# Optimization experiments

Hardware: AMD Instinct MI355X
Metric: run time of the kernel (lower is better)

## Reference

```python
import jax, jax.numpy as jnp
import numpy as np

N = 6            # fixed by nn.Linear(6, h2) after the transpose/squeeze
NEG_SLOPE = 0.01 # F.leaky_relu default


def setup_inputs() -> dict:
    key = jax.random.key(0)
    ks = jax.random.split(key, 12)
    B, H1, H2, H3 = 131072, 64, 512, 256
    in_feat = jax.random.normal(ks[0], (N, B, 1), dtype=jnp.float32)
    # deterministic bidirectional ring: every node has in/out degree 2 (norm='both' safe)
    ar = jnp.arange(N, dtype=jnp.int32)
    src = jnp.concatenate([ar, ar])
    dst = jnp.concatenate([(ar + 1) % N, (ar - 1) % N]).astype(jnp.int32)
    s = 0.2
    W0  = jax.random.normal(ks[1], (1, H1), jnp.float32) * s
    b0  = jax.random.normal(ks[2], (H1,), jnp.float32) * s
    W1  = jax.random.normal(ks[3], (H1, 1), jnp.float32) * s
    b1  = jax.random.normal(ks[4], (1,), jnp.float32) * s
    Wl0 = jax.random.normal(ks[5], (N, H2), jnp.float32) * s
    bl0 = jax.random.normal(ks[6], (H2,), jnp.float32) * s
    Wl2 = jax.random.normal(ks[7], (H2, H3), jnp.float32) * s
    bl2 = jax.random.normal(ks[8], (H3,), jnp.float32) * s
    Wl3 = jax.random.normal(ks[9], (H3, 1), jnp.float32) * s
    bl3 = jax.random.normal(ks[10], (1,), jnp.float32) * s
    return {"in_feat": in_feat, "src": src, "dst": dst,
            "W0": W0, "b0": b0, "W1": W1, "b1": b1,
            "Wl0": Wl0, "bl0": bl0, "Wl2": Wl2, "bl2": bl2,
            "Wl3": Wl3, "bl3": bl3}


def _lrelu(x):
    return jnp.where(x >= 0, x, NEG_SLOPE * x)


def _degree_norms(src, dst):
    ones = jnp.ones(src.shape[0], dtype=jnp.float32)
    deg_out = jax.ops.segment_sum(ones, src, num_segments=N)
    deg_in = jax.ops.segment_sum(ones, dst, num_segments=N)
    return deg_out ** -0.5, deg_in ** -0.5  # DGL GraphConv norm='both'


def _graph_conv(feat, W, b, src, dst, inv_out, inv_in):
    # D_out^{-1/2} A^T D_in^{-1/2} feat  then linear (order is math-equivalent)
    h = feat * inv_out[:, None, None]           # [N,B,F]
    agg = jax.ops.segment_sum(h[src], dst, num_segments=N)  # gather+scatter over edges
    agg = agg * inv_in[:, None, None]
    return agg @ W + b


def reference(in_feat, src, dst, W0, b0, W1, b1, Wl0, bl0, Wl2, bl2, Wl3, bl3):
    inv_out, inv_in = _degree_norms(src, dst)
    h = _lrelu(_graph_conv(in_feat, W0, b0, src, dst, inv_out, inv_in))  # [N,B,h1]
    h = _lrelu(_graph_conv(h, W1, b1, src, dst, inv_out, inv_in))        # [N,B,1]
    x = jnp.transpose(h, (2, 1, 0))[0]   # transpose(0,2).squeeze(0) -> [B,N]
    x = _lrelu(x @ Wl0 + bl0)
    x = _lrelu(x @ Wl2 + bl2)
    x = _lrelu(x @ Wl3 + bl3)            # [B,1]; squeeze(0) is a no-op for B>1
    return x
```

## Files before the change

### kernel.cpp

```cpp
#include <hip/hip_runtime.h>

#define NN   6
#define H1   64
#define H2   512
#define H3   256
#define TM   256
#define KC   32
#define NCH  (H2 / KC)
#define CHUNK_BYTES 32768

typedef short s16x8 __attribute__((ext_vector_type(8)));
typedef float f32x16 __attribute__((ext_vector_type(16)));

__device__ __forceinline__ unsigned short f2bf(float x) {
    unsigned int u = __float_as_uint(x);
    u += 0x7FFFu + ((u >> 16) & 1u);
    return (unsigned short)(u >> 16);
}
__device__ __forceinline__ float bf2f(unsigned short b) {
    return __uint_as_float(((unsigned int)b) << 16);
}
__device__ __forceinline__ void g2lds16(const void* g, void* l) {
    __builtin_amdgcn_global_load_lds(
        (const __attribute__((address_space(1))) unsigned int*)g,
        (__attribute__((address_space(3))) unsigned int*)l, 16, 0, 0);
}

__global__ void split_w(const float* __restrict__ Wl2,
                        unsigned short* __restrict__ Whl) {
    const int tid = blockIdx.x * 256 + threadIdx.x;
    const int c0 = tid >> 13, q = tid & 8191;
    const int j = q & 7, col = (q >> 3) & 255, th = q >> 11;
    const int k = (c0 << 5) + (th << 3) + j;
    const float w = Wl2[k * H3 + col];
    const unsigned short hi = f2bf(w);
    const unsigned short lo = f2bf(w - bf2f(hi));
    Whl[(c0 << 14) + q] = hi;
    Whl[(c0 << 14) + 8192 + q] = lo;
}

__global__ __launch_bounds__(512, 2)
void gcn_mfma(const float* __restrict__ f,
              const float* __restrict__ W0,
              const float* __restrict__ b0,
              const float* __restrict__ W1,
              const float* __restrict__ b1_,
              const float* __restrict__ Wl0,
              const float* __restrict__ bl0,
              const float* __restrict__ bl2,
              const float* __restrict__ Wl3,
              const float* __restrict__ bl3_,
              const unsigned short* __restrict__ Whl,
              float* __restrict__ out,
              int B)
{
    __shared__ float sW0[H1], sB0[H1], sW1[H1];
    __shared__ float sWl0[NN][H2];
    __shared__ float sBl0[H2];
    __shared__ float sBl2[H3];
    __shared__ float sWl3[H3];
    __shared__ float sF[NN][TM];
    __shared__ float sS[NN][TM];
    __shared__ float sX[NN][TM];
    __shared__ __align__(16) unsigned short sB[2][16384];

    const int t    = threadIdx.x;
    const int lane = t & 63;
    const int w    = t >> 6;
    const int cl   = lane & 31;
    const int h    = lane >> 5;
    const int m0   = blockIdx.x * TM;

    for (int i = t; i < H1; i += 512) { sW0[i] = W0[i]; sB0[i] = b0[i]; sW1[i] = W1[i]; }
    for (int i = t; i < NN * H2; i += 512) sWl0[i >> 9][i & (H2 - 1)] = Wl0[i];
    for (int i = t; i < H2; i += 512) sBl0[i] = bl0[i];
    for (int i = t; i < H3; i += 512) { sBl2[i] = bl2[i]; sWl3[i] = Wl3[i]; }
    for (int i = t; i < NN * TM; i += 512) sF[i >> 8][i & 255] = f[(i >> 8) * B + m0 + (i & 255)];

    {
        const char* src = (const char*)Whl + (w << 12) + (lane << 4);
        char*       dst = (char*)&sB[0][0] + (w << 12);
        #pragma unroll
        for (int q = 0; q < 4; ++q) g2lds16(src + (q << 10), dst + (q << 10));
    }
    __syncthreads();

    const float b1v = b1_[0];

    for (int v = t; v < NN * TM; v += 512) {
        const int i = v >> 8, r = v & 255;
        const int im = (i + NN - 1) % NN, ip = (i + 1) % NN;
        const float g = 0.5f * (sF[im][r] + sF[ip][r]);
        float s = 0.f;
        #pragma unroll
        for (int c = 0; c < H1; ++c) {
            float hx = g * sW0[c] + sB0[c];
            hx = fmaxf(hx, 0.01f * hx);
            s += hx * sW1[c];
        }
        sS[i][r] = s;
    }
    __syncthreads();
    for (int v = t; v < NN * TM; v += 512) {
        const int i = v >> 8, r = v & 255;
        const int im = (i + NN - 1) % NN, ip = (i + 1) % NN;
        const float xv = 0.5f * (sS[im][r] + sS[ip][r]) + b1v;
        sX[i][r] = fmaxf(xv, 0.01f * xv);
    }
    __syncthreads();

    const int myrow = (w << 5) + cl;
    const float x0 = sX[0][myrow], x1 = sX[1][myrow], x2 = sX[2][myrow],
                x3 = sX[3][myrow], x4 = sX[4][myrow], x5 = sX[5][myrow];

    f32x16 acc[8];
    #pragma unroll
    for (int c = 0; c < 8; ++c)
        #pragma unroll
        for (int rg = 0; rg < 16; ++rg) acc[c][rg] = 0.f;

    for (int ch = 0; ch < NCH; ++ch) {
        const int cur = ch & 1;
        if (ch + 1 < NCH) {
            const char* src = (const char*)Whl + (ch + 1) * CHUNK_BYTES + (w << 12) + (lane << 4);
            char*       dst = (char*)&sB[cur ^ 1][0] + (w << 12);
            #pragma unroll
            for (int q = 0; q < 4; ++q) g2lds16(src + (q << 10), dst + (q << 10));
        }
        #pragma unroll
        for (int tt = 0; tt < 2; ++tt) {
            const int k0 = (ch << 5) + (tt << 4) + (h << 3);
            float4 va = *(const float4*)&sBl0[k0];
            float4 vb = *(const float4*)&sBl0[k0 + 4];
            #pragma unroll
            for (int i = 0; i < 6; ++i) {
                const float xi = (i == 0) ? x0 : (i == 1) ? x1 : (i == 2) ? x2
                               : (i == 3) ? x3 : (i == 4) ? x4 : x5;
                const float4 wa = *(const float4*)&sWl0[i][k0];
                const float4 wb = *(const float4*)&sWl0[i][k0 + 4];
                va.x += xi * wa.x; va.y += xi * wa.y; va.z += xi * wa.z; va.w += xi * wa.w;
                vb.x += xi * wb.x; vb.y += xi * wb.y; vb.z += xi * wb.z; vb.w += xi * wb.w;
            }
            float vv[8] = {va.x, va.y, va.z, va.w, vb.x, vb.y, vb.z, vb.w};
            s16x8 ah, al;
            #pragma unroll
            for (int j = 0; j < 8; ++j) {
                float v = vv[j];
                v = fmaxf(v, 0.01f * v);
                const unsigned short hb = f2bf(v);
                const unsigned short lb = f2bf(v - bf2f(hb));
                ah[j] = (short)hb;
                al[j] = (short)lb;
            }
            const int thh = (tt << 1) + h;
            s16x8 bh[8];
            #pragma unroll
            for (int c = 0; c < 8; ++c)
                bh[c] = *(const s16x8*)&sB[cur][(((0 + thh) * 256) + (c << 5) + cl) << 3];
            #pragma unroll
            for (int c = 0; c < 8; ++c)
                acc[c] = __builtin_amdgcn_mfma_f32_32x32x16_bf16(ah, bh[c], acc[c], 0, 0, 0);
            #pragma unroll
            for (int c = 0; c < 8; ++c)
                acc[c] = __builtin_amdgcn_mfma_f32_32x32x16_bf16(al, bh[c], acc[c], 0, 0, 0);
            #pragma unroll
            for (int c = 0; c < 8; ++c) {
                const s16x8 bl = *(const s16x8*)&sB[cur][(((4 + thh) * 256) + (c << 5) + cl) << 3];
                acc[c] = __builtin_amdgcn_mfma_f32_32x32x16_bf16(ah, bl, acc[c], 0, 0, 0);
            }
        }
        __syncthreads();
    }

    float ps[16];
    #pragma unroll
    for (int rg = 0; rg < 16; ++rg) ps[rg] = 0.f;
    #pragma unroll
    for (int c = 0; c < 8; ++c) {
        const int col = (c << 5) + cl;
        const float b2 = sBl2[col], w3 = sWl3[col];
        #pragma unroll
        for (int rg = 0; rg < 16; ++rg) {
            float v = acc[c][rg] + b2;
            v = fmaxf(v, 0.01f * v);
            ps[rg] += v * w3;
        }
    }
    #pragma unroll
    for (int m = 1; m < 32; m <<= 1)
        #pragma unroll
        for (int rg = 0; rg < 16; ++rg) ps[rg] += __shfl_xor(ps[rg], m);
    if (cl == 0) {
        const float bl3v = bl3_[0];
        #pragma unroll
        for (int rg = 0; rg < 16; ++rg) {
            const int row = (rg & 3) + ((rg >> 2) << 3) + (h << 2);
            const float v = ps[rg] + bl3v;
            out[m0 + (w << 5) + row] = fmaxf(v, 0.01f * v);
        }
    }
}

extern "C" void kernel_launch(void* const* d_in, const int* in_sizes, int n_in,
                              void* d_out, int out_size, void* d_ws, size_t ws_size,
                              hipStream_t stream) {
    const float* f   = (const float*)d_in[0];
    const float* W0  = (const float*)d_in[3];
    const float* b0  = (const float*)d_in[4];
    const float* W1  = (const float*)d_in[5];
    const float* b1  = (const float*)d_in[6];
    const float* Wl0 = (const float*)d_in[7];
    const float* bl0 = (const float*)d_in[8];
    const float* Wl2 = (const float*)d_in[9];
    const float* bl2 = (const float*)d_in[10];
    const float* Wl3 = (const float*)d_in[11];
    const float* bl3 = (const float*)d_in[12];
    float* out = (float*)d_out;
    unsigned short* Whl = (unsigned short*)d_ws;
    const int B = in_sizes[0] / NN;

    split_w<<<dim3(H2 * H3 / 256), 256, 0, stream>>>(Wl2, Whl);
    gcn_mfma<<<dim3(B / TM), 512, 0, stream>>>(f, W0, b0, W1, b1, Wl0, bl0,
                                               bl2, Wl3, bl3, Whl, out, B);
}
```

Before: 195.0 us.

## Software-pipeline A-fragment generation ahead of MFMAs with packed bf16 conversion

Unrolls the chunk loop by two with fixed double-buffer indices and computes the next chunk's A-operand (first-layer linear, leaky ReLU, hi/lo bf16 split) before issuing the MFMAs for the current chunk. This lets VALU work overlap matrix-core work. It also swaps the scalar bf16 rounding for the packed v_cvt_pk_bf16_f32 instruction and uses 2-wide float vector math. B-fragment loads are split into groups of four to reduce live registers, but the extra prefetched A fragments raise register pressure, which risks occupancy at 2 blocks of 512 threads.

```diff
diff --git a/kernel.cpp b/kernel.cpp
--- a/kernel.cpp
+++ b/kernel.cpp
@@ -11,6 +11,8 @@
 
 typedef short s16x8 __attribute__((ext_vector_type(8)));
 typedef float f32x16 __attribute__((ext_vector_type(16)));
+typedef float f32x2 __attribute__((ext_vector_type(2)));
+typedef unsigned int u32x4 __attribute__((ext_vector_type(4)));
 
 __device__ __forceinline__ unsigned short f2bf(float x) {
     unsigned int u = __float_as_uint(x);
@@ -19,6 +21,11 @@
 }
 __device__ __forceinline__ float bf2f(unsigned short b) {
     return __uint_as_float(((unsigned int)b) << 16);
+}
+__device__ __forceinline__ unsigned int cvt_pk_bf16(float a, float b) {
+    unsigned int r;
+    asm("v_cvt_pk_bf16_f32 %0, %1, %2" : "=v"(r) : "v"(a), "v"(b));
+    return r;
 }
 __device__ __forceinline__ void g2lds16(const void* g, void* l) {
     __builtin_amdgcn_global_load_lds(
@@ -77,12 +84,14 @@
     for (int i = t; i < H3; i += 512) { sBl2[i] = bl2[i]; sWl3[i] = Wl3[i]; }
     for (int i = t; i < NN * TM; i += 512) sF[i >> 8][i & 255] = f[(i >> 8) * B + m0 + (i & 255)];
 
-    {
-        const char* src = (const char*)Whl + (w << 12) + (lane << 4);
-        char*       dst = (char*)&sB[0][0] + (w << 12);
-        #pragma unroll
-        for (int q = 0; q < 4; ++q) g2lds16(src + (q << 10), dst + (q << 10));
-    }
+#define STAGE(CH, BUF) do {                                                        \
+        const char* _src = (const char*)Whl + (CH) * CHUNK_BYTES + (w << 12) + (lane << 4); \
+        char*       _dst = (char*)&sB[BUF][0] + (w << 12);                         \
+        _Pragma("unroll")                                                          \
+        for (int _q = 0; _q < 4; ++_q) g2lds16(_src + (_q << 10), _dst + (_q << 10)); \
+    } while (0)
+
+    STAGE(0, 0);
     __syncthreads();
 
     const float b1v = b1_[0];
@@ -110,8 +119,9 @@
     __syncthreads();
 
     const int myrow = (w << 5) + cl;
-    const float x0 = sX[0][myrow], x1 = sX[1][myrow], x2 = sX[2][myrow],
-                x3 = sX[3][myrow], x4 = sX[4][myrow], x5 = sX[5][myrow];
+    float xr[NN];
+    #pragma unroll
+    for (int i = 0; i < NN; ++i) xr[i] = sX[i][myrow];
 
     f32x16 acc[8];
     #pragma unroll
@@ -119,56 +129,78 @@
         #pragma unroll
         for (int rg = 0; rg < 16; ++rg) acc[c][rg] = 0.f;
 
-    for (int ch = 0; ch < NCH; ++ch) {
-        const int cur = ch & 1;
-        if (ch + 1 < NCH) {
-            const char* src = (const char*)Whl + (ch + 1) * CHUNK_BYTES + (w << 12) + (lane << 4);
-            char*       dst = (char*)&sB[cur ^ 1][0] + (w << 12);
-            #pragma unroll
-            for (int q = 0; q < 4; ++q) g2lds16(src + (q << 10), dst + (q << 10));
-        }
-        #pragma unroll
-        for (int tt = 0; tt < 2; ++tt) {
-            const int k0 = (ch << 5) + (tt << 4) + (h << 3);
-            float4 va = *(const float4*)&sBl0[k0];
-            float4 vb = *(const float4*)&sBl0[k0 + 4];
-            #pragma unroll
-            for (int i = 0; i < 6; ++i) {
-                const float xi = (i == 0) ? x0 : (i == 1) ? x1 : (i == 2) ? x2
-                               : (i == 3) ? x3 : (i == 4) ? x4 : x5;
-                const float4 wa = *(const float4*)&sWl0[i][k0];
-                const float4 wb = *(const float4*)&sWl0[i][k0 + 4];
-                va.x += xi * wa.x; va.y += xi * wa.y; va.z += xi * wa.z; va.w += xi * wa.w;
-                vb.x += xi * wb.x; vb.y += xi * wb.y; vb.z += xi * wb.z; vb.w += xi * wb.w;
-            }
-            float vv[8] = {va.x, va.y, va.z, va.w, vb.x, vb.y, vb.z, vb.w};
-            s16x8 ah, al;
-            #pragma unroll
-            for (int j = 0; j < 8; ++j) {
-                float v = vv[j];
-                v = fmaxf(v, 0.01f * v);
-                const unsigned short hb = f2bf(v);
-                const unsigned short lb = f2bf(v - bf2f(hb));
-                ah[j] = (short)hb;
-                al[j] = (short)lb;
-            }
-            const int thh = (tt << 1) + h;
-            s16x8 bh[8];
-            #pragma unroll
-            for (int c = 0; c < 8; ++c)
-                bh[c] = *(const s16x8*)&sB[cur][(((0 + thh) * 256) + (c << 5) + cl) << 3];
-            #pragma unroll
-            for (int c = 0; c < 8; ++c)
-                acc[c] = __builtin_amdgcn_mfma_f32_32x32x16_bf16(ah, bh[c], acc[c], 0, 0, 0);
-            #pragma unroll
-            for (int c = 0; c < 8; ++c)
-                acc[c] = __builtin_amdgcn_mfma_f32_32x32x16_bf16(al, bh[c], acc[c], 0, 0, 0);
-            #pragma unroll
-            for (int c = 0; c < 8; ++c) {
-                const s16x8 bl = *(const s16x8*)&sB[cur][(((4 + thh) * 256) + (c << 5) + cl) << 3];
-                acc[c] = __builtin_amdgcn_mfma_f32_32x32x16_bf16(ah, bl, acc[c], 0, 0, 0);
-            }
-        }
+#define K0(CH, TT) (((CH) << 5) + ((TT) << 4) + (h << 3))
+#define GEN_TT(K0V, AH, AL) do {                                                   \
+        const int _k0 = (K0V);                                                     \
+        f32x2 _ac[4];                                                              \
+        _Pragma("unroll")                                                          \
+        for (int _j = 0; _j < 4; ++_j) _ac[_j] = *(const f32x2*)&sBl0[_k0 + 2*_j]; \
+        _Pragma("unroll")                                                          \
+        for (int _i = 0; _i < 6; ++_i) {                                           \
+            const float _xi = xr[_i];                                              \
+            _Pragma("unroll")                                                      \
+            for (int _j = 0; _j < 4; ++_j)                                         \
+                _ac[_j] += _xi * (*(const f32x2*)&sWl0[_i][_k0 + 2*_j]);           \
+        }                                                                          \
+        unsigned int _hw[4], _lw[4];                                               \
+        _Pragma("unroll")                                                          \
+        for (int _j = 0; _j < 4; ++_j) {                                           \
+            f32x2 _v = _ac[_j];                                                    \
+            _v = __builtin_elementwise_max(_v, 0.01f * _v);                        \
+            const unsigned int _uh = cvt_pk_bf16(_v[0], _v[1]);                    \
+            f32x2 _hf = { __uint_as_float(_uh << 16),                              \
+                          __uint_as_float(_uh & 0xFFFF0000u) };                    \
+            const f32x2 _r = _v - _hf;                                             \
+            _hw[_j] = _uh; _lw[_j] = cvt_pk_bf16(_r[0], _r[1]);                    \
+        }                                                                          \
+        const u32x4 _u4 = {_hw[0], _hw[1], _hw[2], _hw[3]};                        \
+        const u32x4 _l4 = {_lw[0], _lw[1], _lw[2], _lw[3]};                        \
+        AH = __builtin_bit_cast(s16x8, _u4);                                       \
+        AL = __builtin_bit_cast(s16x8, _l4);                                       \
+    } while (0)
+
+#define MFMA_TT(SBC, TT, AH, AL) do {                                              \
+        const int _thh = ((TT) << 1) + h;                                          \
+        const unsigned short* _bb = &(SBC)[((_thh << 8) + cl) << 3];               \
+        _Pragma("unroll")                                                          \
+        for (int _g = 0; _g < 2; ++_g) {                                           \
+            s16x8 _bh[4];                                                          \
+            _Pragma("unroll")                                                      \
+            for (int _i = 0; _i < 4; ++_i)                                         \
+                _bh[_i] = *(const s16x8*)&_bb[(_g * 4 + _i) << 8];                 \
+            _Pragma("unroll")                                                      \
+            for (int _i = 0; _i < 4; ++_i)                                         \
+                acc[_g*4+_i] = __builtin_amdgcn_mfma_f32_32x32x16_bf16(AH, _bh[_i], acc[_g*4+_i], 0, 0, 0); \
+            _Pragma("unroll")                                                      \
+            for (int _i = 0; _i < 4; ++_i)                                         \
+                acc[_g*4+_i] = __builtin_amdgcn_mfma_f32_32x32x16_bf16(AL, _bh[_i], acc[_g*4+_i], 0, 0, 0); \
+            _Pragma("unroll")                                                      \
+            for (int _i = 0; _i < 4; ++_i) {                                       \
+                const s16x8 _bl = *(const s16x8*)&_bb[8192 + ((_g * 4 + _i) << 8)];\
+                acc[_g*4+_i] = __builtin_amdgcn_mfma_f32_32x32x16_bf16(AH, _bl, acc[_g*4+_i], 0, 0, 0); \
+            }                                                                      \
+        }                                                                          \
+    } while (0)
+
+    s16x8 ahA0, alA0, ahA1, alA1;
+    s16x8 ahB0, alB0, ahB1, alB1;
+    GEN_TT(K0(0, 0), ahA0, alA0);
+    GEN_TT(K0(0, 1), ahA1, alA1);
+
+    for (int ch = 0; ch < NCH; ch += 2) {
+        STAGE(ch + 1, 1);
+        GEN_TT(K0(ch + 1, 0), ahB0, alB0);
+        GEN_TT(K0(ch + 1, 1), ahB1, alB1);
+        MFMA_TT((&sB[0][0]), 0, ahA0, alA0);
+        MFMA_TT((&sB[0][0]), 1, ahA1, alA1);
+        __syncthreads();
+        if (ch + 2 < NCH) {
+            STAGE(ch + 2, 0);
+            GEN_TT(K0(ch + 2, 0), ahA0, alA0);
+            GEN_TT(K0(ch + 2, 1), ahA1, alA1);
+        }
+        MFMA_TT((&sB[1][0]), 0, ahB0, alB0);
+        MFMA_TT((&sB[1][0]), 1, ahB1, alB1);
         __syncthreads();
     }
 
```

Measured after the change: 182.9 us. -6.2%, faster.

## Retile MFMA warps as 2x2 row/col blocks and software-pipeline A-fragment generation

Applied to the files above, without the earlier changes.

Each warp now computes 64 rows by 128 columns instead of 32 rows by 256 columns. This halves the number of A-fragments generated per warp relative to its output work and lets each B-fragment load from LDS feed two MFMAs. The chunk loop is unrolled by two with explicit double buffers, so the layer-1 activations for the next chunk are computed while the current chunk's MFMAs run. The bf16 hi/lo split now uses packed v_cvt_pk_bf16_f32, and split_w reads the weights with float4 loads. The final reduction goes through shared memory across the two column-warps, and the extra live fragments add register pressure.

```diff
diff --git a/kernel.cpp b/kernel.cpp
--- a/kernel.cpp
+++ b/kernel.cpp
@@ -11,6 +11,8 @@
 
 typedef short s16x8 __attribute__((ext_vector_type(8)));
 typedef float f32x16 __attribute__((ext_vector_type(16)));
+typedef float f32x2 __attribute__((ext_vector_type(2)));
+typedef unsigned int u32x4 __attribute__((ext_vector_type(4)));
 
 __device__ __forceinline__ unsigned short f2bf(float x) {
     unsigned int u = __float_as_uint(x);
@@ -20,6 +22,11 @@
 __device__ __forceinline__ float bf2f(unsigned short b) {
     return __uint_as_float(((unsigned int)b) << 16);
 }
+__device__ __forceinline__ unsigned int cvt_pk_bf16(float a, float b) {
+    unsigned int r;
+    asm("v_cvt_pk_bf16_f32 %0, %1, %2" : "=v"(r) : "v"(a), "v"(b));
+    return r;
+}
 __device__ __forceinline__ void g2lds16(const void* g, void* l) {
     __builtin_amdgcn_global_load_lds(
         (const __attribute__((address_space(1))) unsigned int*)g,
@@ -28,15 +35,59 @@
 
 __global__ void split_w(const float* __restrict__ Wl2,
                         unsigned short* __restrict__ Whl) {
-    const int tid = blockIdx.x * 256 + threadIdx.x;
-    const int c0 = tid >> 13, q = tid & 8191;
-    const int j = q & 7, col = (q >> 3) & 255, th = q >> 11;
-    const int k = (c0 << 5) + (th << 3) + j;
-    const float w = Wl2[k * H3 + col];
-    const unsigned short hi = f2bf(w);
-    const unsigned short lo = f2bf(w - bf2f(hi));
-    Whl[(c0 << 14) + q] = hi;
-    Whl[(c0 << 14) + 8192 + q] = lo;
+    const int gid = blockIdx.x * 256 + threadIdx.x;
+    const int k = gid >> 6, c4 = (gid & 63) << 2;
+    const float4 v = *(const float4*)&Wl2[k * H3 + c4];
+    const int c0 = k >> 5, th = (k >> 3) & 3, j = k & 7;
+    const unsigned base = (c0 << 14) + (th << 11) + j;
+    const float vv[4] = {v.x, v.y, v.z, v.w};
+    #pragma unroll
+    for (int c = 0; c < 4; ++c) {
+        const unsigned short hi = f2bf(vv[c]);
+        const unsigned short lo = f2bf(vv[c] - bf2f(hi));
+        Whl[base + ((c4 + c) << 3)] = hi;
+        Whl[base + 8192 + ((c4 + c) << 3)] = lo;
+    }
+}
+
+__device__ __forceinline__ void gen2(const float* sBl0s, const float (*sWl0s)[H2],
+                                     int k0, const float* xr0, const float* xr1,
+                                     s16x8& ah0, s16x8& al0, s16x8& ah1, s16x8& al1)
+{
+    f32x2 a0[4], a1[4];
+    #pragma unroll
+    for (int j = 0; j < 4; ++j) {
+        const f32x2 b = *(const f32x2*)&sBl0s[k0 + 2 * j];
+        f32x2 c0 = b, c1 = b;
+        #pragma unroll
+        for (int i = 0; i < 6; ++i) {
+            const f32x2 wv = *(const f32x2*)&sWl0s[i][k0 + 2 * j];
+            c0 += xr0[i] * wv;
+            c1 += xr1[i] * wv;
+        }
+        a0[j] = c0; a1[j] = c1;
+    }
+    unsigned int h0[4], l0[4], h1[4], l1[4];
+    #pragma unroll
+    for (int j = 0; j < 4; ++j) {
+        f32x2 v = a0[j];
+        v = __builtin_elementwise_max(v, 0.01f * v);
+        unsigned int u = cvt_pk_bf16(v[0], v[1]);
+        f32x2 hf = { __uint_as_float(u << 16), __uint_as_float(u & 0xFFFF0000u) };
+        f32x2 r = v - hf;
+        h0[j] = u; l0[j] = cvt_pk_bf16(r[0], r[1]);
+        v = a1[j];
+        v = __builtin_elementwise_max(v, 0.01f * v);
+        u = cvt_pk_bf16(v[0], v[1]);
+        hf = (f32x2){ __uint_as_float(u << 16), __uint_as_float(u & 0xFFFF0000u) };
+        r = v - hf;
+        h1[j] = u; l1[j] = cvt_pk_bf16(r[0], r[1]);
+    }
+    u32x4 t;
+    t = (u32x4){h0[0], h0[1], h0[2], h0[3]}; ah0 = __builtin_bit_cast(s16x8, t);
+    t = (u32x4){l0[0], l0[1], l0[2], l0[3]}; al0 = __builtin_bit_cast(s16x8, t);
+    t = (u32x4){h1[0], h1[1], h1[2], h1[3]}; ah1 = __builtin_bit_cast(s16x8, t);
+    t = (u32x4){l1[0], l1[1], l1[2], l1[3]}; al1 = __builtin_bit_cast(s16x8, t);
 }
 
 __global__ __launch_bounds__(512, 2)
@@ -64,12 +115,15 @@
     __shared__ float sX[NN][TM];
     __shared__ __align__(16) unsigned short sB[2][16384];
 
-    const int t    = threadIdx.x;
-    const int lane = t & 63;
-    const int w    = t >> 6;
-    const int cl   = lane & 31;
-    const int h    = lane >> 5;
-    const int m0   = blockIdx.x * TM;
+    const int t     = threadIdx.x;
+    const int lane  = t & 63;
+    const int w     = t >> 6;
+    const int cl    = lane & 31;
+    const int h     = lane >> 5;
+    const int wr    = w >> 1;
+    const int wc    = w & 1;
+    const int wc128 = wc << 7;
+    const int m0    = blockIdx.x * TM;
 
     for (int i = t; i < H1; i += 512) { sW0[i] = W0[i]; sB0[i] = b0[i]; sW1[i] = W1[i]; }
     for (int i = t; i < NN * H2; i += 512) sWl0[i >> 9][i & (H2 - 1)] = Wl0[i];
@@ -77,12 +131,14 @@
     for (int i = t; i < H3; i += 512) { sBl2[i] = bl2[i]; sWl3[i] = Wl3[i]; }
     for (int i = t; i < NN * TM; i += 512) sF[i >> 8][i & 255] = f[(i >> 8) * B + m0 + (i & 255)];
 
-    {
-        const char* src = (const char*)Whl + (w << 12) + (lane << 4);
-        char*       dst = (char*)&sB[0][0] + (w << 12);
-        #pragma unroll
-        for (int q = 0; q < 4; ++q) g2lds16(src + (q << 10), dst + (q << 10));
-    }
+#define STAGE(CH, BUF) do {                                                        \
+        const char* _src = (const char*)Whl + (CH) * CHUNK_BYTES + (w << 12) + (lane << 4); \
+        char*       _dst = (char*)&sB[BUF][0] + (w << 12);                         \
+        _Pragma("unroll")                                                          \
+        for (int _q = 0; _q < 4; ++_q) g2lds16(_src + (_q << 10), _dst + (_q << 10)); \
+    } while (0)
+
+    STAGE(0, 0);
     __syncthreads();
 
     const float b1v = b1_[0];
@@ -109,95 +165,102 @@
     }
     __syncthreads();
 
-    const int myrow = (w << 5) + cl;
-    const float x0 = sX[0][myrow], x1 = sX[1][myrow], x2 = sX[2][myrow],
-                x3 = sX[3][myrow], x4 = sX[4][myrow], x5 = sX[5][myrow];
-
-    f32x16 acc[8];
-    #pragma unroll
-    for (int c = 0; c < 8; ++c)
-        #pragma unroll
-        for (int rg = 0; rg < 16; ++rg) acc[c][rg] = 0.f;
-
-    for (int ch = 0; ch < NCH; ++ch) {
-        const int cur = ch & 1;
-        if (ch + 1 < NCH) {
-            const char* src = (const char*)Whl + (ch + 1) * CHUNK_BYTES + (w << 12) + (lane << 4);
-            char*       dst = (char*)&sB[cur ^ 1][0] + (w << 12);
-            #pragma unroll
-            for (int q = 0; q < 4; ++q) g2lds16(src + (q << 10), dst + (q << 10));
-        }
-        #pragma unroll
-        for (int tt = 0; tt < 2; ++tt) {
-            const int k0 = (ch << 5) + (tt << 4) + (h << 3);
-            float4 va = *(const float4*)&sBl0[k0];
-            float4 vb = *(const float4*)&sBl0[k0 + 4];
-            #pragma unroll
-            for (int i = 0; i < 6; ++i) {
-                const float xi = (i == 0) ? x0 : (i == 1) ? x1 : (i == 2) ? x2
-                               : (i == 3) ? x3 : (i == 4) ? x4 : x5;
-                const float4 wa = *(const float4*)&sWl0[i][k0];
-                const float4 wb = *(const float4*)&sWl0[i][k0 + 4];
-                va.x += xi * wa.x; va.y += xi * wa.y; va.z += xi * wa.z; va.w += xi * wa.w;
-                vb.x += xi * wb.x; vb.y += xi * wb.y; vb.z += xi * wb.z; vb.w += xi * wb.w;
+    const int row0 = (wr << 6) + cl;
+    float xr0[NN], xr1[NN];
+    #pragma unroll
+    for (int i = 0; i < NN; ++i) { xr0[i] = sX[i][row0]; xr1[i] = sX[i][row0 + 32]; }
+
+    f32x16 acc[2][4];
+    #pragma unroll
+    for (int m = 0; m < 2; ++m)
+        #pragma unroll
+        for (int n = 0; n < 4; ++n)
+            #pragma unroll
+            for (int rg = 0; rg < 16; ++rg) acc[m][n][rg] = 0.f;
+
+#define K0(CH, TT) (((CH) << 5) + ((TT) << 4) + (h << 3))
+
+#define MFMA_TT(SBC, TT, AH0, AL0, AH1, AL1) do {                                  \
+        const int _thh = ((TT) << 1) + h;                                          \
+        const unsigned short* _bb = &(SBC)[((_thh << 8) + wc128 + cl) << 3];       \
+        s16x8 _bh[4], _bl[4];                                                      \
+        _Pragma("unroll")                                                          \
+        for (int _n = 0; _n < 4; ++_n) {                                           \
+            _bh[_n] = *(const s16x8*)&_bb[_n << 8];                                \
+            _bl[_n] = *(const s16x8*)&_bb[8192 + (_n << 8)];                       \
+        }                                                                          \
+        _Pragma("unroll")                                                          \
+        for (int _n = 0; _n < 4; ++_n) {                                           \
+            acc[0][_n] = __builtin_amdgcn_mfma_f32_32x32x16_bf16(AH0, _bh[_n], acc[0][_n], 0, 0, 0); \
+            acc[1][_n] = __builtin_amdgcn_mfma_f32_32x32x16_bf16(AH1, _bh[_n], acc[1][_n], 0, 0, 0); \
+            acc[0][_n] = __builtin_amdgcn_mfma_f32_32x32x16_bf16(AL0, _bh[_n], acc[0][_n], 0, 0, 0); \
+            acc[1][_n] = __builtin_amdgcn_mfma_f32_32x32x16_bf16(AL1, _bh[_n], acc[1][_n], 0, 0, 0); \
+            acc[0][_n] = __builtin_amdgcn_mfma_f32_32x32x16_bf16(AH0, _bl[_n], acc[0][_n], 0, 0, 0); \
+            acc[1][_n] = __builtin_amdgcn_mfma_f32_32x32x16_bf16(AH1, _bl[_n], acc[1][_n], 0, 0, 0); \
+        }                                                                          \
+    } while (0)
+
+    s16x8 fA[2][4], fB[2][4];
+    gen2(sBl0, sWl0, K0(0, 0), xr0, xr1, fA[0][0], fA[0][1], fA[0][2], fA[0][3]);
+    gen2(sBl0, sWl0, K0(0, 1), xr0, xr1, fA[1][0], fA[1][1], fA[1][2], fA[1][3]);
+
+    for (int ch = 0; ch < NCH; ch += 2) {
+        STAGE(ch + 1, 1);
+        gen2(sBl0, sWl0, K0(ch + 1, 0), xr0, xr1, fB[0][0], fB[0][1], fB[0][2], fB[0][3]);
+        gen2(sBl0, sWl0, K0(ch + 1, 1), xr0, xr1, fB[1][0], fB[1][1], fB[1][2], fB[1][3]);
+        MFMA_TT((&sB[0][0]), 0, fA[0][0], fA[0][1], fA[0][2], fA[0][3]);
+        MFMA_TT((&sB[0][0]), 1, fA[1][0], fA[1][1], fA[1][2], fA[1][3]);
+        __syncthreads();
+        if (ch + 2 < NCH) {
+            STAGE(ch + 2, 0);
+            gen2(sBl0, sWl0, K0(ch + 2, 0), xr0, xr1, fA[0][0], fA[0][1], fA[0][2], fA[0][3]);
+            gen2(sBl0, sWl0, K0(ch + 2, 1), xr0, xr1, fA[1][0], fA[1][1], fA[1][2], fA[1][3]);
+        }
+        MFMA_TT((&sB[1][0]), 0, fB[0][0], fB[0][1], fB[0][2], fB[0][3]);
+        MFMA_TT((&sB[1][0]), 1, fB[1][0], fB[1][1], fB[1][2], fB[1][3]);
+        __syncthreads();
+    }
+
+    float ps[2][16];
+    #pragma unroll
+    for (int m = 0; m < 2; ++m)
+        #pragma unroll
+        for (int rg = 0; rg < 16; ++rg) ps[m][rg] = 0.f;
+    #pragma unroll
+    for (int m = 0; m < 2; ++m)
+        #pragma unroll
+        for (int n = 0; n < 4; ++n) {
+            const int col = wc128 + (n << 5) + cl;
+            const float b2 = sBl2[col], w3 = sWl3[col];
+            #pragma unroll
+            for (int rg = 0; rg < 16; ++rg) {
+                float v = acc[m][n][rg] + b2;
+                v = fmaxf(v, 0.01f * v);
+                ps[m][rg] += v * w3;
             }
-            float vv[8] = {va.x, va.y, va.z, va.w, vb.x, vb.y, vb.z, vb.w};
-            s16x8 ah, al;
-            #pragma unroll
-            for (int j = 0; j < 8; ++j) {
-                float v = vv[j];
-                v = fmaxf(v, 0.01f * v);
-                const unsigned short hb = f2bf(v);
-                const unsigned short lb = f2bf(v - bf2f(hb));
-                ah[j] = (short)hb;
-                al[j] = (short)lb;
+        }
+    #pragma unroll
+    for (int msk = 1; msk < 32; msk <<= 1)
+        #pragma unroll
+        for (int m = 0; m < 2; ++m)
+            #pragma unroll
+            for (int rg = 0; rg < 16; ++rg) ps[m][rg] += __shfl_xor(ps[m][rg], msk);
+
+    float* sRed = &sS[0][0];
+    if (cl == 0) {
+        #pragma unroll
+        for (int m = 0; m < 2; ++m)
+            #pragma unroll
+            for (int rg = 0; rg < 16; ++rg) {
+                const int rowb = (wr << 6) + (m << 5) + (rg & 3) + ((rg >> 2) << 3) + (h << 2);
+                sRed[(wc << 8) + rowb] = ps[m][rg];
             }
-            const int thh = (tt << 1) + h;
-            s16x8 bh[8];
-            #pragma unroll
-            for (int c = 0; c < 8; ++c)
-                bh[c] = *(const s16x8*)&sB[cur][(((0 + thh) * 256) + (c << 5) + cl) << 3];
-            #pragma unroll
-            for (int c = 0; c < 8; ++c)
-                acc[c] = __builtin_amdgcn_mfma_f32_32x32x16_bf16(ah, bh[c], acc[c], 0, 0, 0);
-            #pragma unroll
-            for (int c = 0; c < 8; ++c)
-                acc[c] = __builtin_amdgcn_mfma_f32_32x32x16_bf16(al, bh[c], acc[c], 0, 0, 0);
-            #pragma unroll
-            for (int c = 0; c < 8; ++c) {
-                const s16x8 bl = *(const s16x8*)&sB[cur][(((4 + thh) * 256) + (c << 5) + cl) << 3];
-                acc[c] = __builtin_amdgcn_mfma_f32_32x32x16_bf16(ah, bl, acc[c], 0, 0, 0);
-            }
-        }
-        __syncthreads();
-    }
-
-    float ps[16];
-    #pragma unroll
-    for (int rg = 0; rg < 16; ++rg) ps[rg] = 0.f;
-    #pragma unroll
-    for (int c = 0; c < 8; ++c) {
-        const int col = (c << 5) + cl;
-        const float b2 = sBl2[col], w3 = sWl3[col];
-        #pragma unroll
-        for (int rg = 0; rg < 16; ++rg) {
-            float v = acc[c][rg] + b2;
-            v = fmaxf(v, 0.01f * v);
-            ps[rg] += v * w3;
-        }
-    }
-    #pragma unroll
-    for (int m = 1; m < 32; m <<= 1)
-        #pragma unroll
-        for (int rg = 0; rg < 16; ++rg) ps[rg] += __shfl_xor(ps[rg], m);
-    if (cl == 0) {
+    }
+    __syncthreads();
+    if (t < 256) {
         const float bl3v = bl3_[0];
-        #pragma unroll
-        for (int rg = 0; rg < 16; ++rg) {
-            const int row = (rg & 3) + ((rg >> 2) << 3) + (h << 2);
-            const float v = ps[rg] + bl3v;
-            out[m0 + (w << 5) + row] = fmaxf(v, 0.01f * v);
-        }
+        const float v = sRed[t] + sRed[256 + t] + bl3v;
+        out[m0 + t] = fmaxf(v, 0.01f * v);
     }
 }
 
@@ -219,7 +282,7 @@
     unsigned short* Whl = (unsigned short*)d_ws;
     const int B = in_sizes[0] / NN;
 
-    split_w<<<dim3(H2 * H3 / 256), 256, 0, stream>>>(Wl2, Whl);
+    split_w<<<dim3(128), 256, 0, stream>>>(Wl2, Whl);
     gcn_mfma<<<dim3(B / TM), 512, 0, stream>>>(f, W0, b0, W1, b1, Wl0, bl0,
                                                bl2, Wl3, bl3, Whl, out, B);
 }
```

Result: no change. 194.4 us (-0.3%).
